# Optimization experiments

Measured on AMD Instinct MI355X. Metric: run time of the kernel, lower is better.

The kernel has to match this reference:

```python
import jax, jax.numpy as jnp
import numpy as np

N_NODES = 50000
N_EDGES = 800000
D_NODE = 128
D_EDGE = 16
HID = 128
BN_EPS = 1e-5


def gcn_conv(h, src, dst, W, b):
    # PyG GCNConv: h' = D^-1/2 (A + I) D^-1/2 (h W) + b, deg includes self-loop
    h = h @ W
    deg = jax.ops.segment_sum(jnp.ones((src.shape[0],), h.dtype), dst,
                              num_segments=N_NODES) + 1.0
    dinv = deg ** -0.5
    norm = dinv[src] * dinv[dst]                      # [E]
    agg = jax.ops.segment_sum(h[src] * norm[:, None], dst,
                              num_segments=N_NODES)   # scatter to dst
    agg = agg + h * (dinv * dinv)[:, None]            # self-loop term
    return agg + b


def setup_inputs() -> dict:
    key = jax.random.key(0)
    ks = jax.random.split(key, 12)
    s = lambda fan_in: 1.0 / np.sqrt(fan_in)
    return {
        "x": jax.random.normal(ks[0], (N_NODES, D_NODE), jnp.float32),
        "edge_index": jax.random.randint(ks[1], (2, N_EDGES), 0, N_NODES, jnp.int32),
        "edge_attr": jax.random.normal(ks[2], (N_EDGES, D_EDGE), jnp.float32),
        "W1": jax.random.normal(ks[3], (D_NODE, HID), jnp.float32) * s(D_NODE),
        "b1": jnp.zeros((HID,), jnp.float32),
        "gamma": jnp.ones((HID,), jnp.float32),
        "beta": jnp.zeros((HID,), jnp.float32),
        "W2": jax.random.normal(ks[4], (HID, HID), jnp.float32) * s(HID),
        "b2": jnp.zeros((HID,), jnp.float32),
        "Wm1": jax.random.normal(ks[5], (2 * HID + D_EDGE, HID), jnp.float32) * s(2 * HID + D_EDGE),
        "bm1": jnp.zeros((HID,), jnp.float32),
        "Wm2": jax.random.normal(ks[6], (HID, 1), jnp.float32) * s(HID),
        "bm2": jnp.zeros((1,), jnp.float32),
    }


def reference(x, edge_index, edge_attr, W1, b1, gamma, beta, W2, b2, Wm1, bm1, Wm2, bm2):
    src, dst = edge_index[0], edge_index[1]
    z = gcn_conv(x, src, dst, W1, b1)
    # BatchNorm1d over nodes (training-mode batch stats, biased var)
    mean = jnp.mean(z, axis=0)
    var = jnp.mean(jnp.square(z - mean), axis=0)
    z = (z - mean) * jax.lax.rsqrt(var + BN_EPS) * gamma + beta
    z = jax.nn.relu(z)
    z = gcn_conv(z, src, dst, W2, b2)
    # edge head: gather endpoints, concat with edge_attr, 2-layer MLP (dropout = eval identity)
    edge_input = jnp.concatenate([z[src], z[dst], edge_attr], axis=1)  # [E, 2H+De]
    h = jax.nn.relu(edge_input @ Wm1 + bm1)
    return (h @ Wm2 + bm2).squeeze(-1)  # [E]
```

## Files before the change

kernel.cpp:

```cpp
#include <hip/hip_runtime.h>
#include <hip/hip_bf16.h>

#define NN 50000
#define NE 800000
#define H 128
#define DE 16
#define BN_EPS 1e-5f
#define NB_SCAN 196

typedef float v2f __attribute__((ext_vector_type(2)));
typedef float v4f __attribute__((ext_vector_type(4)));
typedef short bfrag __attribute__((ext_vector_type(8)));

__device__ __forceinline__ unsigned int packbf2(float a, float b) {
    __hip_bfloat162 h = __float22bfloat162_rn(make_float2(a, b));
    return *(unsigned int*)&h;
}
__device__ __forceinline__ v2f unpackbf2(unsigned int u) {
    v2f r;
    r.x = __uint_as_float(u << 16);
    r.y = __uint_as_float(u & 0xffff0000u);
    return r;
}
__device__ __forceinline__ bfrag cvt8(float4 a0, float4 a1) {
    union { uint4 u; bfrag f; } x;
    x.u.x = packbf2(a0.x, a0.y);
    x.u.y = packbf2(a0.z, a0.w);
    x.u.z = packbf2(a1.x, a1.y);
    x.u.w = packbf2(a1.z, a1.w);
    return x.f;
}
#define COMP(u4, j) ((j) == 0 ? (u4).x : (j) == 1 ? (u4).y : (j) == 2 ? (u4).z : (u4).w)

__global__ void hist_k(const int* __restrict__ dst, int* __restrict__ counts) {
    int e = blockIdx.x * 256 + threadIdx.x;
    if (e < NE) atomicAdd(&counts[dst[e]], 1);
}

__global__ void scan1_k(const int* __restrict__ counts, int* __restrict__ bsum) {
    __shared__ int sh[256];
    int i = blockIdx.x * 256 + threadIdx.x;
    int v = (i < NN) ? counts[i] : 0;
    sh[threadIdx.x] = v;
    __syncthreads();
    for (int off = 128; off; off >>= 1) {
        if (threadIdx.x < off) sh[threadIdx.x] += sh[threadIdx.x + off];
        __syncthreads();
    }
    if (!threadIdx.x) bsum[blockIdx.x] = sh[0];
}

__global__ void scan2_k(int* __restrict__ bsum) {
    __shared__ int sh[256];
    int t = threadIdx.x;
    int v = (t < NB_SCAN) ? bsum[t] : 0;
    sh[t] = v;
    __syncthreads();
    for (int off = 1; off < 256; off <<= 1) {
        int x = (t >= off) ? sh[t - off] : 0;
        __syncthreads();
        sh[t] += x;
        __syncthreads();
    }
    if (t < NB_SCAN) bsum[t] = sh[t] - v;
}

__global__ void scan3_k(const int* __restrict__ counts, const int* __restrict__ bsum,
                        int* __restrict__ offsets, int* __restrict__ cursor,
                        float* __restrict__ dinv) {
    __shared__ int sh[256];
    int i = blockIdx.x * 256 + threadIdx.x;
    int v = (i < NN) ? counts[i] : 0;
    sh[threadIdx.x] = v;
    __syncthreads();
    for (int off = 1; off < 256; off <<= 1) {
        int x = (threadIdx.x >= off) ? sh[threadIdx.x - off] : 0;
        __syncthreads();
        sh[threadIdx.x] += x;
        __syncthreads();
    }
    if (i < NN) {
        int excl = sh[threadIdx.x] - v + bsum[blockIdx.x];
        offsets[i] = excl;
        cursor[i] = excl;
        dinv[i] = rsqrtf((float)v + 1.0f);
    }
}

__global__ void fill_k(const int* __restrict__ src, const int* __restrict__ dst,
                       int* __restrict__ cursor, int2* __restrict__ pairs,
                       int* __restrict__ dste) {
    int e = blockIdx.x * 256 + threadIdx.x;
    if (e < NE) {
        int d = dst[e];
        int pos = atomicAdd(&cursor[d], 1);
        pairs[pos] = make_int2(src[e], e);
        dste[pos] = d;
        if (e < 64) pairs[NE + e] = make_int2(0, 0);
    }
}

__global__ void cvtB_k(const float* __restrict__ s0, const float* __restrict__ s1,
                       const float* __restrict__ s2, const float* __restrict__ s3,
                       short* __restrict__ d0, short* __restrict__ d1,
                       short* __restrict__ d2, short* __restrict__ d3) {
    const float* s = blockIdx.y == 0 ? s0 : blockIdx.y == 1 ? s1 : blockIdx.y == 2 ? s2 : s3;
    short* d = blockIdx.y == 0 ? d0 : blockIdx.y == 1 ? d1 : blockIdx.y == 2 ? d2 : d3;
    int idx = blockIdx.x * 256 + threadIdx.x;
    int n = idx & 127, k = idx >> 7;
    float v = s[k * 128 + n];
    d[n * 128 + k] = (short)(packbf2(v, v) & 0xffff);
}

__global__ void cvtWe_k(const float* __restrict__ We, unsigned int* __restrict__ WePk) {
    int idx = blockIdx.x * 256 + threadIdx.x;
    if (idx < 2048) {
        int c = idx >> 8;
        int lane = (idx >> 2) & 63;
        int j2 = (idx & 3) * 2;
        int q = lane >> 4, i = lane & 15;
        int k0 = q * 8 + j2, k1 = k0 + 1;
        int feat = i * 8 + c;
        float v0 = (k0 < 16) ? We[k0 * 128 + feat] : 0.f;
        float v1 = (k1 < 16) ? We[k1 * 128 + feat] : 0.f;
        WePk[idx] = packbf2(v0, v1);
    }
}

__global__ __launch_bounds__(256) void gemm_mfma(const float* __restrict__ A,
                                                 const short* __restrict__ Bt,
                                                 float* __restrict__ C,
                                                 unsigned int* __restrict__ Cb,
                                                 const float* __restrict__ rowScale,
                                                 const float* __restrict__ tA,
                                                 const float* __restrict__ tC,
                                                 int M) {
    int lane = threadIdx.x & 63;
    int w = threadIdx.x >> 6;
    int i = lane & 15;
    int q = lane >> 4;
    int r0 = blockIdx.x * 64 + w * 16;
    int arow = min(r0 + i, M - 1);
    const float* Arow = A + (size_t)arow * 128;

    v4f acc[8];
#pragma unroll
    for (int c = 0; c < 8; c++) acc[c] = (v4f)0.f;

#pragma unroll
    for (int kc = 0; kc < 128; kc += 32) {
        int kb = kc + q * 8;
        float4 a0 = *(const float4*)&Arow[kb];
        float4 a1 = *(const float4*)&Arow[kb + 4];
        if (tA) {
            float4 t0 = *(const float4*)&tA[kb];
            float4 t1 = *(const float4*)&tA[kb + 4];
            float4 c0 = *(const float4*)&tC[kb];
            float4 c1 = *(const float4*)&tC[kb + 4];
            a0.x = fmaxf(a0.x * t0.x + c0.x, 0.f);
            a0.y = fmaxf(a0.y * t0.y + c0.y, 0.f);
            a0.z = fmaxf(a0.z * t0.z + c0.z, 0.f);
            a0.w = fmaxf(a0.w * t0.w + c0.w, 0.f);
            a1.x = fmaxf(a1.x * t1.x + c1.x, 0.f);
            a1.y = fmaxf(a1.y * t1.y + c1.y, 0.f);
            a1.z = fmaxf(a1.z * t1.z + c1.z, 0.f);
            a1.w = fmaxf(a1.w * t1.w + c1.w, 0.f);
        }
        bfrag af = cvt8(a0, a1);
#pragma unroll
        for (int c = 0; c < 8; c++) {
            bfrag bf = *(const bfrag*)&Bt[(size_t)(c * 16 + i) * 128 + kb];
            acc[c] = __builtin_amdgcn_mfma_f32_16x16x32_bf16(af, bf, acc[c], 0, 0, 0);
        }
    }

    int orow0 = r0 + q * 4;
    v4f ds = (v4f)1.f;
    if (rowScale) ds = *(const v4f*)&rowScale[min(orow0, M - 4)];
    if (Cb) {
#pragma unroll
        for (int c = 0; c < 8; c++) {
            int col = c * 16 + i;
#pragma unroll
            for (int r = 0; r < 4; r++) {
                float v = acc[c][r] * ds[r];
                float vp = __shfl_xor(v, 1, 64);
                if (!(i & 1) && orow0 + r < M)
                    Cb[(size_t)(orow0 + r) * 64 + (col >> 1)] = packbf2(v, vp);
            }
        }
    } else {
#pragma unroll
        for (int c = 0; c < 8; c++) {
            int col = c * 16 + i;
#pragma unroll
            for (int r = 0; r < 4; r++) {
                if (orow0 + r < M)
                    C[(size_t)(orow0 + r) * 128 + col] = acc[c][r] * ds[r];
            }
        }
    }
}

__global__ __launch_bounds__(256) void gemm_pq(const unsigned int* __restrict__ zbA,
                                               const short* __restrict__ Bs_,
                                               const short* __restrict__ Bd_,
                                               const float* __restrict__ bm1,
                                               unsigned int* __restrict__ Pb,
                                               unsigned int* __restrict__ Qb,
                                               int M) {
    int lane = threadIdx.x & 63;
    int w = threadIdx.x >> 6;
    int i = lane & 15;
    int q = lane >> 4;
    int r0 = blockIdx.x * 64 + w * 16;
    int arow = min(r0 + i, M - 1);

    v4f accP[8], accQ[8];
#pragma unroll
    for (int c = 0; c < 8; c++) { accP[c] = (v4f)0.f; accQ[c] = (v4f)0.f; }

#pragma unroll
    for (int kc = 0; kc < 128; kc += 32) {
        int kb = kc + q * 8;
        bfrag af = *(const bfrag*)&zbA[(size_t)arow * 64 + (kb >> 1)];
#pragma unroll
        for (int c = 0; c < 8; c++) {
            bfrag bs = *(const bfrag*)&Bs_[(size_t)(c * 16 + i) * 128 + kb];
            bfrag bd = *(const bfrag*)&Bd_[(size_t)(c * 16 + i) * 128 + kb];
            accP[c] = __builtin_amdgcn_mfma_f32_16x16x32_bf16(af, bs, accP[c], 0, 0, 0);
            accQ[c] = __builtin_amdgcn_mfma_f32_16x16x32_bf16(af, bd, accQ[c], 0, 0, 0);
        }
    }

    int orow0 = r0 + q * 4;
    float bm1c[8];
#pragma unroll
    for (int c = 0; c < 8; c++) bm1c[c] = bm1[c * 16 + i];
#pragma unroll
    for (int c = 0; c < 8; c++) {
        int col = c * 16 + i;
#pragma unroll
        for (int r = 0; r < 4; r++) {
            float vP = accP[c][r];
            float vPp = __shfl_xor(vP, 1, 64);
            float vQ = accQ[c][r] + bm1c[c];
            float vQp = __shfl_xor(vQ, 1, 64);
            if (!(i & 1) && orow0 + r < M) {
                Pb[(size_t)(orow0 + r) * 64 + (col >> 1)] = packbf2(vP, vPp);
                Qb[(size_t)(orow0 + r) * 64 + (col >> 1)] = packbf2(vQ, vQp);
            }
        }
    }
}

__global__ __launch_bounds__(256, 8) void aggregate_k(const unsigned int* __restrict__ hsb,
                                                      const int* __restrict__ offsets,
                                                      const int* __restrict__ counts,
                                                      const int2* __restrict__ pairs,
                                                      const float* __restrict__ dinv,
                                                      const float* __restrict__ bias,
                                                      float* __restrict__ zout,
                                                      unsigned int* __restrict__ zbout) {
    int lane = threadIdx.x & 63;
    int n = __builtin_amdgcn_readfirstlane(blockIdx.x * 4 + (threadIdx.x >> 6));
    if (n >= NN) return;
    int beg = offsets[n];
    int cnt = counts[n];
    v2f a0 = {0.f, 0.f}, a1 = {0.f, 0.f}, a2 = {0.f, 0.f}, a3 = {0.f, 0.f};
    v2f a4 = {0.f, 0.f}, a5 = {0.f, 0.f}, a6 = {0.f, 0.f}, a7 = {0.f, 0.f};
    for (int c = 0; c < cnt; c += 64) {
        int vsrc = pairs[beg + c + lane].x;
        int m = min(64, cnt - c);
        int t = 0;
        for (; t + 8 <= m; t += 8) {
            int s0 = __builtin_amdgcn_readlane(vsrc, t);
            int s1 = __builtin_amdgcn_readlane(vsrc, t + 1);
            int s2 = __builtin_amdgcn_readlane(vsrc, t + 2);
            int s3 = __builtin_amdgcn_readlane(vsrc, t + 3);
            int s4 = __builtin_amdgcn_readlane(vsrc, t + 4);
            int s5 = __builtin_amdgcn_readlane(vsrc, t + 5);
            int s6 = __builtin_amdgcn_readlane(vsrc, t + 6);
            int s7 = __builtin_amdgcn_readlane(vsrc, t + 7);
            unsigned int u0 = hsb[(size_t)s0 * 64 + lane];
            unsigned int u1 = hsb[(size_t)s1 * 64 + lane];
            unsigned int u2 = hsb[(size_t)s2 * 64 + lane];
            unsigned int u3 = hsb[(size_t)s3 * 64 + lane];
            unsigned int u4 = hsb[(size_t)s4 * 64 + lane];
            unsigned int u5 = hsb[(size_t)s5 * 64 + lane];
            unsigned int u6 = hsb[(size_t)s6 * 64 + lane];
            unsigned int u7 = hsb[(size_t)s7 * 64 + lane];
            a0 += unpackbf2(u0);
            a1 += unpackbf2(u1);
            a2 += unpackbf2(u2);
            a3 += unpackbf2(u3);
            a4 += unpackbf2(u4);
            a5 += unpackbf2(u5);
            a6 += unpackbf2(u6);
            a7 += unpackbf2(u7);
        }
        for (; t < m; t++) {
            int s0 = __builtin_amdgcn_readlane(vsrc, t);
            a0 += unpackbf2(hsb[(size_t)s0 * 64 + lane]);
        }
    }
    v2f self = unpackbf2(hsb[(size_t)n * 64 + lane]);
    float di = dinv[n];
    int f = lane * 2;
    float2 b = *(const float2*)&bias[f];
    v2f sum = ((a0 + a1) + (a2 + a3)) + ((a4 + a5) + (a6 + a7)) + self;
    float rx = sum.x * di + b.x;
    float ry = sum.y * di + b.y;
    if (zbout) {
        zbout[(size_t)n * 64 + lane] = packbf2(rx, ry);
    } else {
        *(float2*)&zout[(size_t)n * 128 + f] = make_float2(rx, ry);
    }
}

__global__ __launch_bounds__(256) void bnstats_k(const float* __restrict__ z,
                                                 float* __restrict__ sums,
                                                 float* __restrict__ sumsq) {
    __shared__ float ls[128], lq[128];
    int f = threadIdx.x & 127;
    int sub = threadIdx.x >> 7;
    float s = 0.f, q = 0.f;
    for (int r = blockIdx.x * 2 + sub; r < NN; r += gridDim.x * 2) {
        float v = z[(size_t)r * 128 + f];
        s += v;
        q += v * v;
    }
    if (sub) { ls[f] = s; lq[f] = q; }
    __syncthreads();
    if (!sub) {
        atomicAdd(&sums[f], s + ls[f]);
        atomicAdd(&sumsq[f], q + lq[f]);
    }
}

__global__ void bnfinal_k(const float* __restrict__ sums, const float* __restrict__ sumsq,
                          const float* __restrict__ gamma, const float* __restrict__ beta,
                          float* __restrict__ bnA, float* __restrict__ bnC) {
    int f = threadIdx.x;
    if (f < 128) {
        float mean = sums[f] * (1.0f / NN);
        float var = sumsq[f] * (1.0f / NN) - mean * mean;
        float a = gamma[f] * rsqrtf(var + BN_EPS);
        bnA[f] = a;
        bnC[f] = beta[f] - mean * a;
    }
}

__global__ __launch_bounds__(256) void edgehead_k(const unsigned int* __restrict__ Pb,
                                                  const unsigned int* __restrict__ Qb,
                                                  const float* __restrict__ ea,
                                                  const int2* __restrict__ pairs,
                                                  const int* __restrict__ dste,
                                                  const unsigned int* __restrict__ WePk,
                                                  const float* __restrict__ Wm2,
                                                  const float* __restrict__ bm2,
                                                  float* __restrict__ out) {
    int lane = threadIdx.x & 63;
    int wid = threadIdx.x >> 6;
    int base = (blockIdx.x * 4 + wid) * 64;
    int i = lane & 15;
    int q = lane >> 4;

    bfrag wef[8];
#pragma unroll
    for (int c = 0; c < 8; c++)
        wef[c] = *(const bfrag*)&WePk[(c * 64 + lane) * 4];
    float4 wv0 = *(const float4*)&Wm2[i * 8];
    float4 wv1 = *(const float4*)&Wm2[i * 8 + 4];
    float bm2v = bm2[0];

    int2 pr = pairs[base + lane];
    int dv = dste[base + lane];

#pragma unroll
    for (int t = 0; t < 4; t++) {
        int tb = t * 16;
        int eidA = __shfl(pr.y, tb + i, 64);
        bfrag af;
#pragma unroll
        for (int z = 0; z < 8; z++) af[z] = 0;
        if (q < 2) {
            float4 e0 = *(const float4*)&ea[(size_t)eidA * 16 + q * 8];
            float4 e1 = *(const float4*)&ea[(size_t)eidA * 16 + q * 8 + 4];
            af = cvt8(e0, e1);
        }
        uint4 Pu[4], Qu[4];
        int eidw[4];
#pragma unroll
        for (int r = 0; r < 4; r++) {
            int sr = __shfl(pr.x, tb + q * 4 + r, 64);
            int dr = __shfl(dv, tb + q * 4 + r, 64);
            eidw[r] = __shfl(pr.y, tb + q * 4 + r, 64);
            Pu[r] = *(const uint4*)&Pb[(size_t)sr * 64 + i * 4];
            Qu[r] = *(const uint4*)&Qb[(size_t)dr * 64 + i * 4];
        }
        v4f acc[8];
#pragma unroll
        for (int c = 0; c < 8; c++) acc[c] = (v4f)0.f;
#pragma unroll
        for (int c = 0; c < 8; c++)
            acc[c] = __builtin_amdgcn_mfma_f32_16x16x32_bf16(af, wef[c], acc[c], 0, 0, 0);
        float wvp[8] = {wv0.x, wv0.y, wv0.z, wv0.w, wv1.x, wv1.y, wv1.z, wv1.w};
#pragma unroll
        for (int r = 0; r < 4; r++) {
            float s = 0.f;
#pragma unroll
            for (int j = 0; j < 4; j++) {
                v2f pv = unpackbf2(COMP(Pu[r], j));
                v2f qv = unpackbf2(COMP(Qu[r], j));
                float t0 = acc[2 * j][r] + pv.x + qv.x;
                float t1 = acc[2 * j + 1][r] + pv.y + qv.y;
                t0 = fmaxf(t0, 0.f);
                t1 = fmaxf(t1, 0.f);
                s = fmaf(t0, wvp[2 * j], s);
                s = fmaf(t1, wvp[2 * j + 1], s);
            }
#pragma unroll
            for (int off = 1; off <= 8; off <<= 1) s += __shfl_xor(s, off, 64);
            if (i == 0) out[eidw[r]] = s + bm2v;
        }
    }
}

extern "C" void kernel_launch(void* const* d_in, const int* in_sizes, int n_in,
                              void* d_out, int out_size, void* d_ws, size_t ws_size,
                              hipStream_t stream) {
    const float* x     = (const float*)d_in[0];
    const int*   ei    = (const int*)d_in[1];
    const float* ea    = (const float*)d_in[2];
    const float* W1    = (const float*)d_in[3];
    const float* b1    = (const float*)d_in[4];
    const float* gamma = (const float*)d_in[5];
    const float* beta  = (const float*)d_in[6];
    const float* W2    = (const float*)d_in[7];
    const float* b2    = (const float*)d_in[8];
    const float* Wm1   = (const float*)d_in[9];
    const float* bm1   = (const float*)d_in[10];
    const float* Wm2   = (const float*)d_in[11];
    const float* bm2   = (const float*)d_in[12];
    float* out = (float*)d_out;

    const int* srcI = ei;
    const int* dstI = ei + NE;

    char* w = (char*)d_ws;
    auto alloc = [&](size_t bytes) {
        char* p = w;
        w += (bytes + 255) & ~(size_t)255;
        return p;
    };
    float* dinv    = (float*)alloc(NN * 4);
    int*   counts  = (int*)alloc(NN * 4);
    int*   offsets = (int*)alloc(NN * 4);
    int*   cursor  = (int*)alloc(NN * 4);
    int*   bsum    = (int*)alloc(256 * 4);
    int2*  pairs   = (int2*)alloc((size_t)(NE + 64) * 8);
    int*   dste    = (int*)alloc((size_t)NE * 4);
    float* sums    = (float*)alloc(128 * 4);
    float* sumsq   = (float*)alloc(128 * 4);
    float* bnA     = (float*)alloc(128 * 4);
    float* bnC     = (float*)alloc(128 * 4);
    short* bt1     = (short*)alloc(128 * 128 * 2);
    short* bt2     = (short*)alloc(128 * 128 * 2);
    short* bts     = (short*)alloc(128 * 128 * 2);
    short* btd     = (short*)alloc(128 * 128 * 2);
    unsigned int* WePk = (unsigned int*)alloc(2048 * 4);
    unsigned int* hsb  = (unsigned int*)alloc((size_t)NN * 64 * 4);
    float* bufZ    = (float*)alloc((size_t)NN * 128 * 4);
    unsigned int* zb2 = (unsigned int*)bufZ;
    unsigned int* Qb  = (unsigned int*)bufZ + (size_t)NN * 64;

    hipMemsetAsync(counts, 0, NN * 4, stream);
    hipMemsetAsync(sums, 0, 128 * 4, stream);
    hipMemsetAsync(sumsq, 0, 128 * 4, stream);

    hist_k<<<(NE + 255) / 256, 256, 0, stream>>>(dstI, counts);
    scan1_k<<<NB_SCAN, 256, 0, stream>>>(counts, bsum);
    scan2_k<<<1, 256, 0, stream>>>(bsum);
    scan3_k<<<NB_SCAN, 256, 0, stream>>>(counts, bsum, offsets, cursor, dinv);
    fill_k<<<(NE + 255) / 256, 256, 0, stream>>>(srcI, dstI, cursor, pairs, dste);
    cvtB_k<<<dim3(64, 4), 256, 0, stream>>>(W1, W2, Wm1, Wm1 + 128 * 128,
                                            bt1, bt2, bts, btd);
    cvtWe_k<<<8, 256, 0, stream>>>(Wm1 + 256 * 128, WePk);

    const int GB = (NN + 63) / 64;
    const int AGG = (NN + 3) / 4;

    gemm_mfma<<<GB, 256, 0, stream>>>(x, bt1, nullptr, hsb, dinv, nullptr, nullptr, NN);
    aggregate_k<<<AGG, 256, 0, stream>>>(hsb, offsets, counts, pairs, dinv, b1, bufZ, nullptr);

    bnstats_k<<<256, 256, 0, stream>>>(bufZ, sums, sumsq);
    bnfinal_k<<<1, 128, 0, stream>>>(sums, sumsq, gamma, beta, bnA, bnC);

    gemm_mfma<<<GB, 256, 0, stream>>>(bufZ, bt2, nullptr, hsb, dinv, bnA, bnC, NN);
    aggregate_k<<<AGG, 256, 0, stream>>>(hsb, offsets, counts, pairs, dinv, b2, nullptr, zb2);

    gemm_pq<<<GB, 256, 0, stream>>>(zb2, bts, btd, bm1, hsb, Qb, NN);

    edgehead_k<<<NE / 256, 256, 0, stream>>>(hsb, Qb, ea, pairs, dste, WePk,
                                             Wm2, bm2, out);
}
```

Measured before the change: 467.7 us.

## Process edge head in original edge order and shrink CSR to source-only array

The edge head now walks edges in their original order, reading src/dst straight from edge_index and edge_attr rows contiguously with nontemporal loads, and writes outputs contiguously with nontemporal stores. This replaces the gathered edge_attr reads and scattered output writes that came from dst-sorted order. The CSR fill now stores only source indices (4 bytes per edge instead of 12), which cuts fill write traffic and aggregate index reads. The cost is that P/Q gathers by dst lose the locality dst-sorted order gave them.

```diff
diff --git a/kernel.cpp b/kernel.cpp
--- a/kernel.cpp
+++ b/kernel.cpp
@@ -23,6 +23,14 @@
     return r;
 }
 __device__ __forceinline__ bfrag cvt8(float4 a0, float4 a1) {
+    union { uint4 u; bfrag f; } x;
+    x.u.x = packbf2(a0.x, a0.y);
+    x.u.y = packbf2(a0.z, a0.w);
+    x.u.z = packbf2(a1.x, a1.y);
+    x.u.w = packbf2(a1.z, a1.w);
+    return x.f;
+}
+__device__ __forceinline__ bfrag cvt8v(v4f a0, v4f a1) {
     union { uint4 u; bfrag f; } x;
     x.u.x = packbf2(a0.x, a0.y);
     x.u.y = packbf2(a0.z, a0.w);
@@ -88,15 +96,12 @@
 }
 
 __global__ void fill_k(const int* __restrict__ src, const int* __restrict__ dst,
-                       int* __restrict__ cursor, int2* __restrict__ pairs,
-                       int* __restrict__ dste) {
+                       int* __restrict__ cursor, int* __restrict__ srcs) {
     int e = blockIdx.x * 256 + threadIdx.x;
     if (e < NE) {
         int d = dst[e];
         int pos = atomicAdd(&cursor[d], 1);
-        pairs[pos] = make_int2(src[e], e);
-        dste[pos] = d;
-        if (e < 64) pairs[NE + e] = make_int2(0, 0);
+        srcs[pos] = src[e];
     }
 }
 
@@ -257,7 +262,7 @@
 __global__ __launch_bounds__(256, 8) void aggregate_k(const unsigned int* __restrict__ hsb,
                                                       const int* __restrict__ offsets,
                                                       const int* __restrict__ counts,
-                                                      const int2* __restrict__ pairs,
+                                                      const int* __restrict__ srcs,
                                                       const float* __restrict__ dinv,
                                                       const float* __restrict__ bias,
                                                       float* __restrict__ zout,
@@ -270,7 +275,7 @@
     v2f a0 = {0.f, 0.f}, a1 = {0.f, 0.f}, a2 = {0.f, 0.f}, a3 = {0.f, 0.f};
     v2f a4 = {0.f, 0.f}, a5 = {0.f, 0.f}, a6 = {0.f, 0.f}, a7 = {0.f, 0.f};
     for (int c = 0; c < cnt; c += 64) {
-        int vsrc = pairs[beg + c + lane].x;
+        int vsrc = srcs[beg + c + lane];
         int m = min(64, cnt - c);
         int t = 0;
         for (; t + 8 <= m; t += 8) {
@@ -354,8 +359,8 @@
 __global__ __launch_bounds__(256) void edgehead_k(const unsigned int* __restrict__ Pb,
                                                   const unsigned int* __restrict__ Qb,
                                                   const float* __restrict__ ea,
-                                                  const int2* __restrict__ pairs,
-                                                  const int* __restrict__ dste,
+                                                  const int* __restrict__ srcI,
+                                                  const int* __restrict__ dstI,
                                                   const unsigned int* __restrict__ WePk,
                                                   const float* __restrict__ Wm2,
                                                   const float* __restrict__ bm2,
@@ -374,28 +379,26 @@
     float4 wv1 = *(const float4*)&Wm2[i * 8 + 4];
     float bm2v = bm2[0];
 
-    int2 pr = pairs[base + lane];
-    int dv = dste[base + lane];
+    int sv = srcI[base + lane];
+    int dv = dstI[base + lane];
 
 #pragma unroll
     for (int t = 0; t < 4; t++) {
         int tb = t * 16;
-        int eidA = __shfl(pr.y, tb + i, 64);
         bfrag af;
 #pragma unroll
         for (int z = 0; z < 8; z++) af[z] = 0;
         if (q < 2) {
-            float4 e0 = *(const float4*)&ea[(size_t)eidA * 16 + q * 8];
-            float4 e1 = *(const float4*)&ea[(size_t)eidA * 16 + q * 8 + 4];
-            af = cvt8(e0, e1);
+            const float* erow = &ea[(size_t)(base + tb + i) * 16 + q * 8];
+            v4f e0 = __builtin_nontemporal_load((const v4f*)erow);
+            v4f e1 = __builtin_nontemporal_load((const v4f*)(erow + 4));
+            af = cvt8v(e0, e1);
         }
         uint4 Pu[4], Qu[4];
-        int eidw[4];
 #pragma unroll
         for (int r = 0; r < 4; r++) {
-            int sr = __shfl(pr.x, tb + q * 4 + r, 64);
+            int sr = __shfl(sv, tb + q * 4 + r, 64);
             int dr = __shfl(dv, tb + q * 4 + r, 64);
-            eidw[r] = __shfl(pr.y, tb + q * 4 + r, 64);
             Pu[r] = *(const uint4*)&Pb[(size_t)sr * 64 + i * 4];
             Qu[r] = *(const uint4*)&Qb[(size_t)dr * 64 + i * 4];
         }
@@ -422,7 +425,7 @@
             }
 #pragma unroll
             for (int off = 1; off <= 8; off <<= 1) s += __shfl_xor(s, off, 64);
-            if (i == 0) out[eidw[r]] = s + bm2v;
+            if (i == 0) __builtin_nontemporal_store(s + bm2v, &out[base + tb + q * 4 + r]);
         }
     }
 }
@@ -459,8 +462,7 @@
     int*   offsets = (int*)alloc(NN * 4);
     int*   cursor  = (int*)alloc(NN * 4);
     int*   bsum    = (int*)alloc(256 * 4);
-    int2*  pairs   = (int2*)alloc((size_t)(NE + 64) * 8);
-    int*   dste    = (int*)alloc((size_t)NE * 4);
+    int*   srcs    = (int*)alloc((size_t)(NE + 64) * 4);
     float* sums    = (float*)alloc(128 * 4);
     float* sumsq   = (float*)alloc(128 * 4);
     float* bnA     = (float*)alloc(128 * 4);
@@ -483,7 +485,7 @@
     scan1_k<<<NB_SCAN, 256, 0, stream>>>(counts, bsum);
     scan2_k<<<1, 256, 0, stream>>>(bsum);
     scan3_k<<<NB_SCAN, 256, 0, stream>>>(counts, bsum, offsets, cursor, dinv);
-    fill_k<<<(NE + 255) / 256, 256, 0, stream>>>(srcI, dstI, cursor, pairs, dste);
+    fill_k<<<(NE + 255) / 256, 256, 0, stream>>>(srcI, dstI, cursor, srcs);
     cvtB_k<<<dim3(64, 4), 256, 0, stream>>>(W1, W2, Wm1, Wm1 + 128 * 128,
                                             bt1, bt2, bts, btd);
     cvtWe_k<<<8, 256, 0, stream>>>(Wm1 + 256 * 128, WePk);
@@ -492,16 +494,16 @@
     const int AGG = (NN + 3) / 4;
 
     gemm_mfma<<<GB, 256, 0, stream>>>(x, bt1, nullptr, hsb, dinv, nullptr, nullptr, NN);
-    aggregate_k<<<AGG, 256, 0, stream>>>(hsb, offsets, counts, pairs, dinv, b1, bufZ, nullptr);
+    aggregate_k<<<AGG, 256, 0, stream>>>(hsb, offsets, counts, srcs, dinv, b1, bufZ, nullptr);
 
     bnstats_k<<<256, 256, 0, stream>>>(bufZ, sums, sumsq);
     bnfinal_k<<<1, 128, 0, stream>>>(sums, sumsq, gamma, beta, bnA, bnC);
 
     gemm_mfma<<<GB, 256, 0, stream>>>(bufZ, bt2, nullptr, hsb, dinv, bnA, bnC, NN);
-    aggregate_k<<<AGG, 256, 0, stream>>>(hsb, offsets, counts, pairs, dinv, b2, nullptr, zb2);
+    aggregate_k<<<AGG, 256, 0, stream>>>(hsb, offsets, counts, srcs, dinv, b2, nullptr, zb2);
 
     gemm_pq<<<GB, 256, 0, stream>>>(zb2, bts, btd, bm1, hsb, Qb, NN);
 
-    edgehead_k<<<NE / 256, 256, 0, stream>>>(hsb, Qb, ea, pairs, dste, WePk,
+    edgehead_k<<<NE / 256, 256, 0, stream>>>(hsb, Qb, ea, srcI, dstI, WePk,
                                              Wm2, bm2, out);
 }
```

New measurement: 463.5 us. Within noise of the previous version (-0.9%).
